# Performance work log

Measured on AMD Instinct MI355X. Metric: run time of the kernel, lower is better.

The kernel has to match this reference:

```python
import jax, jax.numpy as jnp
import numpy as np
import math

EPS = 1e-6  # PCEN eps


def _logit(p):
    return math.log(p / (1.0 - p))


def _pcen(mel, log_s, log_alpha, log_delta, log_r, dmin, dmax):
    """PCEN: per-channel energy normalization. mel: (B, M, T); params: (M,)."""
    s = jnp.clip(jax.nn.sigmoid(log_s), 0.05, 0.3)            # (M,)
    alpha = jnp.clip(jax.nn.sigmoid(log_alpha), 0.9, 0.999)   # (M,)
    delta = jnp.clip(jnp.exp(log_delta), dmin, dmax)          # (M,)
    r = jnp.clip(jax.nn.sigmoid(log_r), 0.05, 0.25)           # (M,)

    # IIR smoother over time: smoother_0 = mel[..., 0];
    # for t in 0..T-1: smoother = (1-s)*smoother + s*mel_t  (t=0 included -> smoothed_0 = mel_0)
    mel_t = jnp.transpose(mel, (2, 0, 1))  # (T, B, M)

    def step(sm, x):
        sm = (1.0 - s) * sm + s * x
        return sm, sm

    _, smoothed_t = jax.lax.scan(step, mel_t[0], mel_t)
    smoothed = jnp.transpose(smoothed_t, (1, 2, 0))  # (B, M, T)

    gain = (EPS + smoothed) ** (-alpha[None, :, None])
    d = delta[None, :, None]
    rr = r[None, :, None]
    return (mel * gain + d) ** rr - d ** rr


def setup_inputs() -> dict:
    key = jax.random.key(0)
    B, M, T = 64, 80, 4000
    mel = jax.random.uniform(key, (B, M, T), dtype=jnp.float32)
    f = jnp.full
    return {
        "mel": mel,
        # non-stationary expert PCEN (s=0.025, alpha=0.99, delta=2.0, r=0.5)
        "log_s_ns": f((M,), _logit(0.025), jnp.float32),
        "log_alpha_ns": f((M,), _logit(0.99), jnp.float32),
        "log_delta_ns": f((M,), math.log(2.0), jnp.float32),
        "log_r_ns": f((M,), _logit(0.5), jnp.float32),
        # stationary expert PCEN (s=0.15, alpha=0.99, delta=0.01, r=0.1)
        "log_s_st": f((M,), _logit(0.15), jnp.float32),
        "log_alpha_st": f((M,), _logit(0.99), jnp.float32),
        "log_delta_st": f((M,), math.log(0.01), jnp.float32),
        "log_r_st": f((M,), _logit(0.1), jnp.float32),
        "gate_temp": jnp.asarray(5.0, jnp.float32),
    }


def reference(mel, log_s_ns, log_alpha_ns, log_delta_ns, log_r_ns,
              log_s_st, log_alpha_st, log_delta_st, log_r_st, gate_temp):
    out_ns = _pcen(mel, log_s_ns, log_alpha_ns, log_delta_ns, log_r_ns, 0.5, 5.0)
    out_st = _pcen(mel, log_s_st, log_alpha_st, log_delta_st, log_r_st, 0.001, 0.1)

    # routing signal: spectral flatness + spectral tilt (0 learnable params)
    log_mel = jnp.log(mel + 1e-8)
    geo = jnp.exp(jnp.mean(log_mel, axis=1, keepdims=True))          # (B,1,T)
    arith = jnp.mean(mel, axis=1, keepdims=True) + 1e-8
    sf = jnp.clip(geo / arith, 0.0, 1.0)

    M = mel.shape[1]
    low = jnp.mean(mel[:, : M // 3, :], axis=1, keepdims=True)
    high = jnp.mean(mel[:, 2 * M // 3 :, :], axis=1, keepdims=True)
    tilt = jnp.clip(low / (low + high + 1e-8), 0.0, 1.0)

    sf_adj = sf + (1.0 - sf) * jax.nn.relu(tilt - 0.6)
    gate = jax.nn.sigmoid(gate_temp * (sf_adj - 0.5))
    return gate * out_st + (1.0 - gate) * out_ns
```

## Files before the change

kernel.cpp:

```cpp
#include <hip/hip_runtime.h>
#include <math.h>

static constexpr int kM = 80;
static constexpr int kT = 4000;
static constexpr int kB = 64;
static constexpr int kLow = kM / 3;
static constexpr int kHighStart = 2 * kM / 3;
static constexpr int kHighCount = kM - kHighStart;
static constexpr int kTrunc = 12;
#define EPSF 1e-6f
#define LOG2E 1.4426950408889634f

typedef float vfloat4 __attribute__((ext_vector_type(4)));
typedef float vfloat2 __attribute__((ext_vector_type(2)));

__device__ __forceinline__ float hw_exp2(float x) { return __builtin_amdgcn_exp2f(x); }
__device__ __forceinline__ float hw_log2(float x) { return __builtin_amdgcn_logf(x); }

__device__ __forceinline__ float fast_sigmoid(float x) {
    return __builtin_amdgcn_rcpf(1.0f + hw_exp2(-x * LOG2E));
}

__global__ __launch_bounds__(256, 4) void gate_kernel(
    const float* __restrict__ mel,
    const float* __restrict__ gate_temp,
    float* __restrict__ gate)
{
    const int lane = threadIdx.x & 63;
    const int wid  = threadIdx.x >> 6;
    const int b    = blockIdx.y;
    const int t0   = blockIdx.x * 256 + lane * 4;
    const bool valid = (t0 < kT);

    const float* base = mel + (size_t)b * kM * kT + t0;
    const int m0 = wid * 20;

    vfloat4 slog = {0.f,0.f,0.f,0.f}, ssum = {0.f,0.f,0.f,0.f};
    vfloat4 slow = {0.f,0.f,0.f,0.f}, shigh = {0.f,0.f,0.f,0.f};

    if (valid) {
        vfloat4 v[20];
        #pragma unroll
        for (int j = 0; j < 20; ++j) {
            v[j] = *reinterpret_cast<const vfloat4*>(base + (size_t)(m0 + j) * kT);
        }
        #pragma unroll
        for (int j = 0; j < 20; ++j) {
            const int m = m0 + j;
            vfloat4 lg;
            lg.x = hw_log2(v[j].x + 1e-8f); lg.y = hw_log2(v[j].y + 1e-8f);
            lg.z = hw_log2(v[j].z + 1e-8f); lg.w = hw_log2(v[j].w + 1e-8f);
            slog += lg;
            ssum += v[j];
            if (m < kLow)        slow  += v[j];
            if (m >= kHighStart) shigh += v[j];
        }
    }

    __shared__ vfloat4 sh[4][4][64];
    sh[wid][0][lane] = slog;
    sh[wid][1][lane] = ssum;
    sh[wid][2][lane] = slow;
    sh[wid][3][lane] = shigh;
    __syncthreads();

    if (wid == 0 && valid) {
        slog  = sh[0][0][lane] + sh[1][0][lane] + sh[2][0][lane] + sh[3][0][lane];
        ssum  = sh[0][1][lane] + sh[1][1][lane] + sh[2][1][lane] + sh[3][1][lane];
        slow  = sh[0][2][lane] + sh[1][2][lane] + sh[2][2][lane] + sh[3][2][lane];
        shigh = sh[0][3][lane] + sh[1][3][lane] + sh[2][3][lane] + sh[3][3][lane];

        const float gt = gate_temp[0];
        vfloat4 o;
        #pragma unroll
        for (int q = 0; q < 4; ++q) {
            const float sl = slog[q];
            const float ss = ssum[q];
            const float lo = slow[q];
            const float hi = shigh[q];
            const float geo   = hw_exp2(sl * (1.0f / kM));
            const float arith = ss * (1.0f / kM) + 1e-8f;
            float sf = geo * __builtin_amdgcn_rcpf(arith);
            sf = fminf(fmaxf(sf, 0.0f), 1.0f);
            const float low  = lo * (1.0f / kLow);
            const float high = hi * (1.0f / kHighCount);
            float tilt = low * __builtin_amdgcn_rcpf(low + high + 1e-8f);
            tilt = fminf(fmaxf(tilt, 0.0f), 1.0f);
            const float sfa = sf + (1.0f - sf) * fmaxf(tilt - 0.6f, 0.0f);
            o[q] = fast_sigmoid(gt * (sfa - 0.5f));
        }
        *reinterpret_cast<vfloat4*>(gate + (size_t)b * kT + t0) = o;
    }
}

__global__ __launch_bounds__(256) void pcen_kernel(
    const float* __restrict__ mel,
    const float* __restrict__ ls_ns, const float* __restrict__ la_ns,
    const float* __restrict__ ld_ns, const float* __restrict__ lr_ns,
    const float* __restrict__ ls_st, const float* __restrict__ la_st,
    const float* __restrict__ ld_st, const float* __restrict__ lr_st,
    const float* __restrict__ gate,
    float* __restrict__ out)
{
    const int m = blockIdx.x;
    const int b = blockIdx.y;

    const float s_ns     = fminf(fmaxf(fast_sigmoid(ls_ns[m]), 0.05f), 0.3f);
    const float alpha_ns = fminf(fmaxf(fast_sigmoid(la_ns[m]), 0.9f), 0.999f);
    const float delta_ns = fminf(fmaxf(hw_exp2(ld_ns[m] * LOG2E), 0.5f), 5.0f);
    const float r_ns     = fminf(fmaxf(fast_sigmoid(lr_ns[m]), 0.05f), 0.25f);
    const float s_st     = fminf(fmaxf(fast_sigmoid(ls_st[m]), 0.05f), 0.3f);
    const float alpha_st = fminf(fmaxf(fast_sigmoid(la_st[m]), 0.9f), 0.999f);
    const float delta_st = fminf(fmaxf(hw_exp2(ld_st[m] * LOG2E), 0.001f), 0.1f);
    const float r_st     = fminf(fmaxf(fast_sigmoid(lr_st[m]), 0.05f), 0.25f);
    const float dr_ns = hw_exp2(r_ns * hw_log2(delta_ns));
    const float dr_st = hw_exp2(r_st * hw_log2(delta_st));

    const vfloat2 a2 = {1.0f - s_ns, 1.0f - s_st};
    const vfloat2 s2 = {s_ns, s_st};
    const vfloat2 d2 = {delta_ns, delta_st};
    const float man = -alpha_ns, mas = -alpha_st;

    const size_t rowoff = ((size_t)b * kM + m) * kT;
    const float* row = mel + rowoff;

    const int i  = threadIdx.x;
    const int t0 = i * 16;
    const bool valid = (t0 < kT);

    float x[16];
    float gv[16];
    if (valid) {
        const float4* p = reinterpret_cast<const float4*>(row + t0);
        #pragma unroll
        for (int q = 0; q < 4; ++q) {
            const float4 v = p[q];
            x[4*q+0] = v.x; x[4*q+1] = v.y; x[4*q+2] = v.z; x[4*q+3] = v.w;
        }
        const float4* gp = reinterpret_cast<const float4*>(gate + (size_t)b * kT + t0);
        #pragma unroll
        for (int q = 0; q < 4; ++q) {
            const float4 v = gp[q];
            gv[4*q+0] = v.x; gv[4*q+1] = v.y; gv[4*q+2] = v.z; gv[4*q+3] = v.w;
        }
    } else {
        #pragma unroll
        for (int k = 0; k < 16; ++k) { x[k] = 0.0f; gv[k] = 0.0f; }
    }

    __shared__ float sv0;
    if (i == 0) sv0 = x[0];

    vfloat2 Bv = {0.0f, 0.0f};
    #pragma unroll
    for (int k = 0; k < 16; ++k) {
        Bv = a2 * Bv + s2 * x[k];
    }
    const vfloat2 p2  = a2 * a2;
    const vfloat2 p4  = p2 * p2;
    const vfloat2 p8  = p4 * p4;
    const vfloat2 A2  = p8 * p8;

    __shared__ vfloat2 Btab[256];
    Btab[i] = Bv;
    __syncthreads();

    vfloat2 sm = {0.0f, 0.0f};
    vfloat2 pw = {1.0f, 1.0f};
    #pragma unroll
    for (int k = 0; k < kTrunc; ++k) {
        const vfloat2 Bk = Btab[(i - 1 - k) & 255];
        if (k < i) {
            sm = pw * Bk + sm;
            pw = pw * A2;
        }
    }
    if (i <= kTrunc) {
        const float x0 = sv0;
        const vfloat2 x02 = {x0, x0};
        sm = pw * x02 + sm;
    }

    if (valid) {
        float4* op = reinterpret_cast<float4*>(out + rowoff + t0);
        #pragma unroll
        for (int q = 0; q < 4; ++q) {
            float4 v;
            #pragma unroll
            for (int j = 0; j < 4; ++j) {
                const int k = 4*q + j;
                const float xv = x[k];
                sm = a2 * sm + s2 * xv;
                vfloat2 g2;
                g2.x = hw_exp2(man * hw_log2(sm.x + EPSF));
                g2.y = hw_exp2(mas * hw_log2(sm.y + EPSF));
                const vfloat2 u2 = g2 * xv + d2;
                const float on = hw_exp2(r_ns * hw_log2(u2.x)) - dr_ns;
                const float os = hw_exp2(r_st * hw_log2(u2.y)) - dr_st;
                (&v.x)[j] = fmaf(gv[k], os - on, on);
            }
            op[q] = v;
        }
    }
}

extern "C" void kernel_launch(void* const* d_in, const int* in_sizes, int n_in,
                              void* d_out, int out_size, void* d_ws, size_t ws_size,
                              hipStream_t stream)
{
    const float* mel       = (const float*)d_in[0];
    const float* ls_ns     = (const float*)d_in[1];
    const float* la_ns     = (const float*)d_in[2];
    const float* ld_ns     = (const float*)d_in[3];
    const float* lr_ns     = (const float*)d_in[4];
    const float* ls_st     = (const float*)d_in[5];
    const float* la_st     = (const float*)d_in[6];
    const float* ld_st     = (const float*)d_in[7];
    const float* lr_st     = (const float*)d_in[8];
    const float* gate_temp = (const float*)d_in[9];
    float* out  = (float*)d_out;
    float* gate = (float*)d_ws;

    dim3 gA(16, kB);
    gate_kernel<<<gA, 256, 0, stream>>>(mel, gate_temp, gate);

    dim3 gB(kM, kB);
    pcen_kernel<<<gB, 256, 0, stream>>>(mel, ls_ns, la_ns, ld_ns, lr_ns,
                                        ls_st, la_st, ld_st, lr_st, gate, out);
}
```

Before: 181.2 us.

## Split each PCEN row across two 128-thread blocks with truncated warm-up

The PCEN kernel now processes each (b,m) row in two halves, each handled by a 128-thread block, instead of one 256-thread block in which only 250 threads were active. The second half rebuilds its starting IIR state by scanning the 12 chunks just before its boundary, reusing the same truncation already used for the in-block scan. This is meant to cut the idle lanes in each block and give the scheduler smaller, more numerous blocks. The cost is a few extra global loads and a short warm-up recurrence in the second half, which relies on the truncation error staying negligible.

```diff
diff --git a/kernel.cpp b/kernel.cpp
--- a/kernel.cpp
+++ b/kernel.cpp
@@ -8,6 +8,8 @@
 static constexpr int kHighStart = 2 * kM / 3;
 static constexpr int kHighCount = kM - kHighStart;
 static constexpr int kTrunc = 12;
+static constexpr int kHalf = kT / 2;
+static constexpr int kChunksPerHalf = kHalf / 16;
 #define EPSF 1e-6f
 #define LOG2E 1.4426950408889634f
 
@@ -74,16 +76,12 @@
         vfloat4 o;
         #pragma unroll
         for (int q = 0; q < 4; ++q) {
-            const float sl = slog[q];
-            const float ss = ssum[q];
-            const float lo = slow[q];
-            const float hi = shigh[q];
-            const float geo   = hw_exp2(sl * (1.0f / kM));
-            const float arith = ss * (1.0f / kM) + 1e-8f;
+            const float geo   = hw_exp2(slog[q] * (1.0f / kM));
+            const float arith = ssum[q] * (1.0f / kM) + 1e-8f;
             float sf = geo * __builtin_amdgcn_rcpf(arith);
             sf = fminf(fmaxf(sf, 0.0f), 1.0f);
-            const float low  = lo * (1.0f / kLow);
-            const float high = hi * (1.0f / kHighCount);
+            const float low  = slow[q]  * (1.0f / kLow);
+            const float high = shigh[q] * (1.0f / kHighCount);
             float tilt = low * __builtin_amdgcn_rcpf(low + high + 1e-8f);
             tilt = fminf(fmaxf(tilt, 0.0f), 1.0f);
             const float sfa = sf + (1.0f - sf) * fmaxf(tilt - 0.6f, 0.0f);
@@ -93,7 +91,7 @@
     }
 }
 
-__global__ __launch_bounds__(256) void pcen_kernel(
+__global__ __launch_bounds__(128) void pcen_kernel(
     const float* __restrict__ mel,
     const float* __restrict__ ls_ns, const float* __restrict__ la_ns,
     const float* __restrict__ ld_ns, const float* __restrict__ lr_ns,
@@ -102,8 +100,9 @@
     const float* __restrict__ gate,
     float* __restrict__ out)
 {
-    const int m = blockIdx.x;
-    const int b = blockIdx.y;
+    const int half = blockIdx.x;
+    const int m    = blockIdx.y;
+    const int b    = blockIdx.z;
 
     const float s_ns     = fminf(fmaxf(fast_sigmoid(ls_ns[m]), 0.05f), 0.3f);
     const float alpha_ns = fminf(fmaxf(fast_sigmoid(la_ns[m]), 0.9f), 0.999f);
@@ -124,9 +123,14 @@
     const size_t rowoff = ((size_t)b * kM + m) * kT;
     const float* row = mel + rowoff;
 
-    const int i  = threadIdx.x;
-    const int t0 = i * 16;
-    const bool valid = (t0 < kT);
+    const int i      = threadIdx.x;
+    const int tstart = half * kHalf;
+    const int t0     = tstart + i * 16;
+    const bool valid = (i < kChunksPerHalf);
+
+    __shared__ float  sv0;
+    __shared__ vfloat2 Btab[kChunksPerHalf];
+    __shared__ vfloat2 warmB[kTrunc];
 
     float x[16];
     float gv[16];
@@ -143,45 +147,63 @@
             const float4 v = gp[q];
             gv[4*q+0] = v.x; gv[4*q+1] = v.y; gv[4*q+2] = v.z; gv[4*q+3] = v.w;
         }
-    } else {
-        #pragma unroll
-        for (int k = 0; k < 16; ++k) { x[k] = 0.0f; gv[k] = 0.0f; }
-    }
-
-    __shared__ float sv0;
-    if (i == 0) sv0 = x[0];
+    }
+
+    if (half == 0 && i == 0) sv0 = x[0];
+
+    if (half == 1 && i < kTrunc) {
+        const float4* wp = reinterpret_cast<const float4*>(row + tstart - kTrunc * 16 + i * 16);
+        vfloat2 wB = {0.0f, 0.0f};
+        #pragma unroll
+        for (int q = 0; q < 4; ++q) {
+            const float4 v = wp[q];
+            wB = a2 * wB + s2 * v.x;
+            wB = a2 * wB + s2 * v.y;
+            wB = a2 * wB + s2 * v.z;
+            wB = a2 * wB + s2 * v.w;
+        }
+        warmB[i] = wB;
+    }
 
     vfloat2 Bv = {0.0f, 0.0f};
-    #pragma unroll
-    for (int k = 0; k < 16; ++k) {
-        Bv = a2 * Bv + s2 * x[k];
+    if (valid) {
+        #pragma unroll
+        for (int k = 0; k < 16; ++k) {
+            Bv = a2 * Bv + s2 * x[k];
+        }
+        Btab[i] = Bv;
     }
     const vfloat2 p2  = a2 * a2;
     const vfloat2 p4  = p2 * p2;
     const vfloat2 p8  = p4 * p4;
     const vfloat2 A2  = p8 * p8;
 
-    __shared__ vfloat2 Btab[256];
-    Btab[i] = Bv;
     __syncthreads();
 
-    vfloat2 sm = {0.0f, 0.0f};
-    vfloat2 pw = {1.0f, 1.0f};
-    #pragma unroll
-    for (int k = 0; k < kTrunc; ++k) {
-        const vfloat2 Bk = Btab[(i - 1 - k) & 255];
-        if (k < i) {
-            sm = pw * Bk + sm;
-            pw = pw * A2;
-        }
-    }
-    if (i <= kTrunc) {
-        const float x0 = sv0;
-        const vfloat2 x02 = {x0, x0};
-        sm = pw * x02 + sm;
-    }
-
-    if (valid) {
+    if (valid) {
+        vfloat2 sm = {0.0f, 0.0f};
+        vfloat2 pw = {1.0f, 1.0f};
+        #pragma unroll
+        for (int k = 0; k < kTrunc; ++k) {
+            if (k < i) {
+                sm = pw * Btab[i - 1 - k] + sm;
+                pw = pw * A2;
+            }
+        }
+        if (i <= kTrunc) {
+            vfloat2 C2;
+            if (half == 0) {
+                C2.x = sv0; C2.y = sv0;
+            } else {
+                C2.x = 0.0f; C2.y = 0.0f;
+                #pragma unroll
+                for (int j = 0; j < kTrunc; ++j) {
+                    C2 = A2 * C2 + warmB[j];
+                }
+            }
+            sm = pw * C2 + sm;
+        }
+
         float4* op = reinterpret_cast<float4*>(out + rowoff + t0);
         #pragma unroll
         for (int q = 0; q < 4; ++q) {
@@ -224,7 +246,7 @@
     dim3 gA(16, kB);
     gate_kernel<<<gA, 256, 0, stream>>>(mel, gate_temp, gate);
 
-    dim3 gB(kM, kB);
-    pcen_kernel<<<gB, 256, 0, stream>>>(mel, ls_ns, la_ns, ld_ns, lr_ns,
+    dim3 gB(2, kM, kB);
+    pcen_kernel<<<gB, 128, 0, stream>>>(mel, ls_ns, la_ns, ld_ns, lr_ns,
                                         ls_st, la_st, ld_st, lr_st, gate, out);
 }
```

Result: no change. 183.8 us (+1.4%).
